# Optimization experiments

Hardware: AMD Instinct MI355X
Metric: run time of the kernel (lower is better)

The kernel has to match this reference:

```python
import jax, jax.numpy as jnp
import numpy as np

MARGIN = 0.5  # init kwarg 'margin'
TWO_N, D = 8192, 256


def setup_inputs() -> dict:
    key = jax.random.key(0)
    k1, k2 = jax.random.split(key)
    embeddings = jax.random.normal(k1, (TWO_N, D), dtype=jnp.float32)
    neg_mask = jax.random.bernoulli(k2, 0.5, (TWO_N, TWO_N))  # bool [2N, 2N]
    return {"embeddings": embeddings, "neg_mask": neg_mask}


def _cdist(x, y):
    # Euclidean pairwise distances via the Gram trick (matches torch.cdist p=2)
    x2 = jnp.sum(x * x, axis=-1)[:, None]
    y2 = jnp.sum(y * y, axis=-1)[None, :]
    sq = jnp.maximum(x2 + y2 - 2.0 * (x @ y.T), 0.0)
    return jnp.sqrt(sq + 1e-12)


def reference(embeddings, neg_mask):
    two_n = embeddings.shape[0]
    n = two_n // 2
    d = _cdist(embeddings, embeddings)  # [2N, 2N]
    # masked sum of exp(margin - d) per anchor row (vectorizes the python loop)
    exp_neg = jnp.where(neg_mask, jnp.exp(MARGIN - d), 0.0)
    row_sums = exp_neg.sum(axis=1)  # [2N]
    idx = jnp.arange(n)
    ap = d[idx, idx + n]  # anchor-positive distances [N]
    j = jnp.log(row_sums[:n] + row_sums[n:]) + ap  # [N]
    # original skips NaN entries before the mean
    valid = ~jnp.isnan(j)
    r2 = jnp.where(valid, jnp.square(jnp.maximum(j, 0.0)), 0.0)
    cnt = jnp.maximum(valid.sum(), 1).astype(r2.dtype)
    loss = r2.sum() / cnt / 2.0
    return loss
```

## Files before the change

kernel.cpp:

```cpp
#include <hip/hip_runtime.h>
#include <hip/hip_bf16.h>
#include <stdint.h>

#define TWO_N  8192
#define NHALF  4096
#define DDIM   256
#define MARGIN 0.5f
#define NTRI   2080

static const size_t OFF_EMB  = 0;
static const size_t OFF_X2   = 4u * 1024 * 1024;
static const size_t OFF_AP   = OFF_X2 + (size_t)TWO_N * 4;
static const size_t OFF_FLAG = OFF_AP + (size_t)NHALF * 4;
static const size_t OFF_PART = OFF_FLAG + 256;
static const size_t OFF_RS   = OFF_PART + 64ull * TWO_N * 4;

typedef __attribute__((ext_vector_type(8))) short bf16x8;
typedef __attribute__((ext_vector_type(4))) float f32x4;

__device__ inline ushort f2bf(float f) {
  uint32_t u = __float_as_uint(f);
  uint32_t r = (u + 0x7FFFu + ((u >> 16) & 1u)) >> 16;
  return (ushort)r;
}
__device__ inline float bf2f(ushort h) { return __uint_as_float((uint32_t)h << 16); }

__device__ inline void gload_lds16(const void* g, void* l) {
  __builtin_amdgcn_global_load_lds(
      (const __attribute__((address_space(1))) uint32_t*)(uintptr_t)g,
      (__attribute__((address_space(3))) uint32_t*)(uint32_t)(uintptr_t)l,
      16, 0, 0);
}

__global__ __launch_bounds__(256) void smv2_prep(
    const float* __restrict__ emb,
    const uint32_t* __restrict__ maskw,
    ushort* __restrict__ emb_bf,
    float* __restrict__ x2,
    int* __restrict__ flag)
{
  const int t = threadIdx.x;
  if (blockIdx.x == 0) {
    __shared__ int sflag;
    if (t == 0) sflag = 0;
    __syncthreads();
    int found = 0;
    #pragma unroll
    for (int k = 0; k < 8; ++k) {
      uint32_t w = maskw[t * 8 + k];
      if (w > 1u && (w & 0xFEFEFEFEu) == 0u) found = 1;
    }
    if (found) atomicOr(&sflag, 1);
    __syncthreads();
    if (t == 0) *flag = sflag;
  }
  const int row  = blockIdx.x * 8 + (t >> 5);
  const int lane = t & 31;
  const float* rp = emb + (size_t)row * DDIM + lane * 8;
  float4 v0 = *(const float4*)(rp);
  float4 v1 = *(const float4*)(rp + 4);
  float vals[8] = {v0.x, v0.y, v0.z, v0.w, v1.x, v1.y, v1.z, v1.w};
  uint32_t packed[4];
  float ss = 0.f;
  #pragma unroll
  for (int k = 0; k < 4; ++k) {
    ushort h0 = f2bf(vals[2 * k]);
    ushort h1 = f2bf(vals[2 * k + 1]);
    packed[k] = (uint32_t)h0 | ((uint32_t)h1 << 16);
    float f0 = bf2f(h0), f1 = bf2f(h1);
    ss += f0 * f0 + f1 * f1;
  }
  *(uint4*)(emb_bf + (size_t)row * DDIM + lane * 8) =
      make_uint4(packed[0], packed[1], packed[2], packed[3]);
  #pragma unroll
  for (int m = 1; m < 32; m <<= 1) ss += __shfl_xor(ss, m);
  if (lane == 0) x2[row] = ss;
}

__global__ __launch_bounds__(512, 6) void smv2_main(
    const ushort* __restrict__ emb_bf,
    const float* __restrict__ x2,
    const uint8_t* __restrict__ mask8,
    const int* __restrict__ flagp,
    float* __restrict__ ap,
    float* __restrict__ partial)
{
  __shared__ char ldsA[128 * 128];
  __shared__ char ldsB[128 * 128];
  __shared__ uint8_t ldsM[128 * 128];
  __shared__ float ldsX[256];

  const int t = threadIdx.x;

  const int bid = blockIdx.x;
  const int idx = (bid & 7) * (NTRI / 8) + (bid >> 3);
  float rf = sqrtf(8.f * (float)idx + 1.f);
  int bx = (int)((rf - 1.f) * 0.5f);
  while ((bx + 1) * (bx + 2) / 2 <= idx) ++bx;
  while (bx * (bx + 1) / 2 > idx) --bx;
  const int by = idx - bx * (bx + 1) / 2;
  const int brow = by * 128;
  const int bcol = bx * 128;
  const bool diag = (bx == by);

  const char* gA = (const char*)(emb_bf + (size_t)brow * DDIM);
  const char* gB = (const char*)(emb_bf + (size_t)bcol * DDIM);

  #pragma unroll
  for (int it = 0; it < 2; ++it) {
    const int dl   = it * 8192 + t * 16;
    const int mrow = dl >> 7;
    const int mc   = dl & 127;
    const int msw  = ((mrow >> 2) & 3) << 5;
    gload_lds16(mask8 + (size_t)(brow + mrow) * TWO_N + bcol + (mc ^ msw), ldsM + dl);
  }
  if (t < 64) {
    const float* src = (t < 32) ? (x2 + brow + t * 4) : (x2 + bcol + (t - 32) * 4);
    gload_lds16(src, (char*)ldsX + t * 16);
  }
  #pragma unroll
  for (int it = 0; it < 2; ++it) {
    const int dl  = it * 8192 + t * 16;
    const int row = dl >> 7;
    const int c   = dl & 127;
    const int cb  = c ^ ((row & 7) << 4);
    gload_lds16(gA + (size_t)row * 512 + cb, ldsA + dl);
    gload_lds16(gB + (size_t)row * 512 + cb, ldsB + dl);
  }
  __syncthreads();

  const int w  = t >> 6;
  const int l  = t & 63;
  const int wr = w >> 2;
  const int wc = w & 3;
  const int cl = l & 15;
  const int kh = l >> 4;
  const int swz = (cl & 7) << 4;

  f32x4 acc[4][2];
  #pragma unroll
  for (int m = 0; m < 4; ++m)
    #pragma unroll
    for (int n = 0; n < 2; ++n) {
      f32x4 z = {0.f, 0.f, 0.f, 0.f};
      acc[m][n] = z;
    }

  #pragma unroll
  for (int p = 0; p < 4; ++p) {
    #pragma unroll
    for (int ks = 0; ks < 2; ++ks) {
      const int kb = ks * 64 + kh * 16;
      bf16x8 a[4], b[2];
      #pragma unroll
      for (int m = 0; m < 4; ++m)
        a[m] = *(const bf16x8*)(ldsA + (wr * 64 + m * 16 + cl) * 128 + (kb ^ swz));
      #pragma unroll
      for (int n = 0; n < 2; ++n)
        b[n] = *(const bf16x8*)(ldsB + (wc * 32 + n * 16 + cl) * 128 + (kb ^ swz));
      #pragma unroll
      for (int m = 0; m < 4; ++m)
        #pragma unroll
        for (int n = 0; n < 2; ++n)
          acc[m][n] = __builtin_amdgcn_mfma_f32_16x16x32_bf16(a[m], b[n], acc[m][n], 0, 0, 0);
    }
    __syncthreads();
    if (p < 3) {
      #pragma unroll
      for (int it = 0; it < 2; ++it) {
        const int dl  = it * 8192 + t * 16;
        const int row = dl >> 7;
        const int c   = dl & 127;
        const int cb  = c ^ ((row & 7) << 4);
        gload_lds16(gA + (size_t)row * 512 + (p + 1) * 128 + cb, ldsA + dl);
        gload_lds16(gB + (size_t)row * 512 + (p + 1) * 128 + cb, ldsB + dl);
      }
      __syncthreads();
    }
  }

  const int isByte = *flagp;
  const uint32_t* maskww = (const uint32_t*)mask8;

  uint32_t m2r[2][4];
  if (!diag && isByte) {
    #pragma unroll
    for (int n = 0; n < 2; ++n) {
      const int gj = bcol + wc * 32 + n * 16 + cl;
      #pragma unroll
      for (int m = 0; m < 4; ++m)
        m2r[n][m] = *(const uint32_t*)(mask8 + (size_t)gj * TWO_N + brow + wr * 64 + m * 16 + kh * 4);
    }
  }

  float* part  = (float*)ldsA;
  float* part2 = (float*)ldsB;
  float cs[2] = {0.f, 0.f};

  #pragma unroll
  for (int m = 0; m < 4; ++m) {
    #pragma unroll
    for (int q = 0; q < 4; ++q) {
      const int lrow = wr * 64 + m * 16 + kh * 4 + q;
      const int gi = brow + lrow;
      const float xi = ldsX[lrow];
      const int msw = kh << 5;
      float rp = 0.f;
      #pragma unroll
      for (int n = 0; n < 2; ++n) {
        const int jc = wc * 32 + n * 16 + cl;
        const int gj = bcol + jc;
        const float g = acc[m][n][q];
        float sq = (gi == gj) ? 0.f : (xi + ldsX[128 + jc] - 2.f * g);
        sq = fmaxf(sq, 0.f) + 1e-12f;
        const float dd = sqrtf(sq);
        if (gj == gi + NHALF && gi < NHALF) ap[gi] = dd;
        const float e = __expf(MARGIN - dd);
        bool mk1;
        if (isByte) mk1 = ldsM[lrow * 128 + (jc ^ msw)] != 0;
        else        mk1 = maskww[(size_t)gi * TWO_N + gj] != 0u;
        rp += mk1 ? e : 0.f;
        if (!diag) {
          bool mk2;
          if (isByte) mk2 = ((m2r[n][m] >> (8 * q)) & 255u) != 0u;
          else        mk2 = maskww[(size_t)gj * TWO_N + gi] != 0u;
          cs[n] += mk2 ? e : 0.f;
        }
      }
      #pragma unroll
      for (int s = 1; s < 16; s <<= 1) rp += __shfl_xor(rp, s);
      if (cl == 0) part[wc * 128 + lrow] = rp;
    }
  }

  if (!diag) {
    #pragma unroll
    for (int n = 0; n < 2; ++n) {
      cs[n] += __shfl_xor(cs[n], 16);
      cs[n] += __shfl_xor(cs[n], 32);
      if (l < 16) part2[wr * 128 + wc * 32 + n * 16 + l] = cs[n];
    }
  }
  __syncthreads();

  if (t < 128) {
    partial[(size_t)bx * TWO_N + brow + t] =
        (part[t] + part[128 + t]) + (part[256 + t] + part[384 + t]);
    if (!diag)
      partial[(size_t)by * TWO_N + bcol + t] = part2[t] + part2[128 + t];
  }
}

__global__ __launch_bounds__(256) void smv2_rowsum(
    const float* __restrict__ partial, float* __restrict__ rs)
{
  const int row = blockIdx.x * 256 + threadIdx.x;
  float s = 0.f;
  #pragma unroll 8
  for (int b = 0; b < 64; ++b) s += partial[(size_t)b * TWO_N + row];
  rs[row] = s;
}

__global__ __launch_bounds__(1024) void smv2_finalize(
    const float* __restrict__ rs, const float* __restrict__ ap,
    float* __restrict__ out)
{
  const int t = threadIdx.x;
  float sum = 0.f, cnt = 0.f;
  for (int i = t; i < NHALF; i += 1024) {
    float rsum = rs[i] + rs[i + NHALF];
    float jv = logf(rsum) + ap[i];
    if (!isnan(jv)) {
      cnt += 1.f;
      float mj = fmaxf(jv, 0.f);
      sum += mj * mj;
    }
  }
  __shared__ float ssum[16], scnt[16];
  #pragma unroll
  for (int s = 32; s >= 1; s >>= 1) {
    sum += __shfl_down(sum, s);
    cnt += __shfl_down(cnt, s);
  }
  const int wid = t >> 6, lid = t & 63;
  if (lid == 0) { ssum[wid] = sum; scnt[wid] = cnt; }
  __syncthreads();
  if (t == 0) {
    float S = 0.f, C = 0.f;
    #pragma unroll
    for (int i = 0; i < 16; ++i) { S += ssum[i]; C += scnt[i]; }
    if (C < 1.f) C = 1.f;
    out[0] = S / C * 0.5f;
  }
}

extern "C" void kernel_launch(void* const* d_in, const int* in_sizes, int n_in,
                              void* d_out, int out_size, void* d_ws, size_t ws_size,
                              hipStream_t stream) {
  const float* emb = (const float*)d_in[0];
  const void* mask = d_in[1];
  char* ws = (char*)d_ws;

  ushort* emb_bf = (ushort*)(ws + OFF_EMB);
  float*  x2     = (float*)(ws + OFF_X2);
  float*  ap     = (float*)(ws + OFF_AP);
  int*    flag   = (int*)(ws + OFF_FLAG);
  float*  part   = (float*)(ws + OFF_PART);
  float*  rs     = (float*)(ws + OFF_RS);

  smv2_prep<<<1024, 256, 0, stream>>>(emb, (const uint32_t*)mask, emb_bf, x2, flag);
  smv2_main<<<NTRI, 512, 0, stream>>>(emb_bf, x2, (const uint8_t*)mask, flag, ap, part);
  smv2_rowsum<<<32, 256, 0, stream>>>(part, rs);
  smv2_finalize<<<1, 1024, 0, stream>>>(rs, ap, (float*)d_out);
}
```

Measured before the change: 455.6 us.

## Pipeline the K-loop with a three-stage LDS ring and explicit vmcnt waits

Replaces the four-step K loop, which loaded a 128-wide chunk and then waited on full barriers, with eight 32-wide phases. The phases use a three-buffer LDS ring filled by direct global-to-LDS loads, with hand-tuned s_waitcnt vmcnt counts so loads overlap the MFMA work. The transposed mask loads move inside the pipeline, and sqrt becomes the raw hardware builtin. The occupancy hint drops from 6 to 4 to leave room for the extra LDS and registers. The risks are lost occupancy, fragile hand-counted waits, and transposed mask loads that now run even on diagonal tiles.

```diff
diff --git a/kernel.cpp b/kernel.cpp
--- a/kernel.cpp
+++ b/kernel.cpp
@@ -31,6 +31,9 @@
       (__attribute__((address_space(3))) uint32_t*)(uint32_t)(uintptr_t)l,
       16, 0, 0);
 }
+
+#define STR2(x) #x
+#define WAITVM(N) asm volatile("s_waitcnt vmcnt(" STR2(N) ")" ::: "memory")
 
 __global__ __launch_bounds__(256) void smv2_prep(
     const float* __restrict__ emb,
@@ -77,7 +80,7 @@
   if (lane == 0) x2[row] = ss;
 }
 
-__global__ __launch_bounds__(512, 6) void smv2_main(
+__global__ __launch_bounds__(512, 4) void smv2_main(
     const ushort* __restrict__ emb_bf,
     const float* __restrict__ x2,
     const uint8_t* __restrict__ mask8,
@@ -85,8 +88,8 @@
     float* __restrict__ ap,
     float* __restrict__ partial)
 {
-  __shared__ char ldsA[128 * 128];
-  __shared__ char ldsB[128 * 128];
+  __shared__ char bufA[3 * 8192];
+  __shared__ char bufB[3 * 8192];
   __shared__ uint8_t ldsM[128 * 128];
   __shared__ float ldsX[256];
 
@@ -106,6 +109,92 @@
   const char* gA = (const char*)(emb_bf + (size_t)brow * DDIM);
   const char* gB = (const char*)(emb_bf + (size_t)bcol * DDIM);
 
+  const int srow = t >> 2;
+  const int scb  = ((t & 3) * 16) ^ (((srow >> 1) & 3) << 4);
+  const size_t gAoff = (size_t)srow * 512 + scb;
+  const size_t gBoff = gAoff;
+  const int ldst = t * 16;
+
+  const int w  = t >> 6;
+  const int l  = t & 63;
+  const int wr = w >> 2;
+  const int wc = w & 3;
+  const int cl = l & 15;
+  const int kh = l >> 4;
+
+  int aoff[4], boff[2];
+  #pragma unroll
+  for (int m = 0; m < 4; ++m) {
+    const int row = wr * 64 + m * 16 + cl;
+    aoff[m] = row * 64 + ((kh * 16) ^ (((row >> 1) & 3) << 4));
+  }
+  #pragma unroll
+  for (int n = 0; n < 2; ++n) {
+    const int row = wc * 32 + n * 16 + cl;
+    boff[n] = row * 64 + ((kh * 16) ^ (((row >> 1) & 3) << 4));
+  }
+
+  f32x4 acc[4][2];
+  #pragma unroll
+  for (int m = 0; m < 4; ++m)
+    #pragma unroll
+    for (int n = 0; n < 2; ++n) {
+      f32x4 z = {0.f, 0.f, 0.f, 0.f};
+      acc[m][n] = z;
+    }
+  uint32_t m2r[2][4];
+
+#define STAGE(Q)                                                            \
+  {                                                                         \
+    gload_lds16(gA + gAoff + (Q) * 64, bufA + ((Q) % 3) * 8192 + ldst);     \
+    gload_lds16(gB + gBoff + (Q) * 64, bufB + ((Q) % 3) * 8192 + ldst);     \
+  }
+
+#define M2LOAD                                                              \
+  {                                                                         \
+    _Pragma("unroll")                                                       \
+    for (int n = 0; n < 2; ++n) {                                           \
+      const int gj = bcol + wc * 32 + n * 16 + cl;                          \
+      _Pragma("unroll")                                                     \
+      for (int m = 0; m < 4; ++m)                                           \
+        m2r[n][m] = *(const uint32_t*)(mask8 + (size_t)gj * TWO_N + brow +  \
+                                       wr * 64 + m * 16 + kh * 4);          \
+    }                                                                       \
+  }
+
+#define COMPUTE(P)                                                          \
+  {                                                                         \
+    const char* ba = bufA + ((P) % 3) * 8192;                               \
+    const char* bb = bufB + ((P) % 3) * 8192;                               \
+    bf16x8 a0 = *(const bf16x8*)(ba + aoff[0]);                             \
+    bf16x8 a1 = *(const bf16x8*)(ba + aoff[1]);                             \
+    bf16x8 a2 = *(const bf16x8*)(ba + aoff[2]);                             \
+    bf16x8 a3 = *(const bf16x8*)(ba + aoff[3]);                             \
+    bf16x8 b0 = *(const bf16x8*)(bb + boff[0]);                             \
+    bf16x8 b1 = *(const bf16x8*)(bb + boff[1]);                             \
+    acc[0][0] = __builtin_amdgcn_mfma_f32_16x16x32_bf16(a0, b0, acc[0][0], 0, 0, 0); \
+    acc[0][1] = __builtin_amdgcn_mfma_f32_16x16x32_bf16(a0, b1, acc[0][1], 0, 0, 0); \
+    acc[1][0] = __builtin_amdgcn_mfma_f32_16x16x32_bf16(a1, b0, acc[1][0], 0, 0, 0); \
+    acc[1][1] = __builtin_amdgcn_mfma_f32_16x16x32_bf16(a1, b1, acc[1][1], 0, 0, 0); \
+    acc[2][0] = __builtin_amdgcn_mfma_f32_16x16x32_bf16(a2, b0, acc[2][0], 0, 0, 0); \
+    acc[2][1] = __builtin_amdgcn_mfma_f32_16x16x32_bf16(a2, b1, acc[2][1], 0, 0, 0); \
+    acc[3][0] = __builtin_amdgcn_mfma_f32_16x16x32_bf16(a3, b0, acc[3][0], 0, 0, 0); \
+    acc[3][1] = __builtin_amdgcn_mfma_f32_16x16x32_bf16(a3, b1, acc[3][1], 0, 0, 0); \
+  }
+
+#define PHASE(P, NW, SQ, DOM2)                                              \
+  {                                                                         \
+    WAITVM(NW);                                                             \
+    __builtin_amdgcn_s_barrier();                                           \
+    __builtin_amdgcn_sched_barrier(0);                                      \
+    if ((SQ) >= 0) STAGE((SQ) < 0 ? 0 : (SQ));                              \
+    if (DOM2) M2LOAD;                                                       \
+    __builtin_amdgcn_sched_barrier(0);                                      \
+    COMPUTE(P);                                                             \
+  }
+
+  STAGE(0);
+  STAGE(1);
   #pragma unroll
   for (int it = 0; it < 2; ++it) {
     const int dl   = it * 8192 + t * 16;
@@ -114,87 +203,25 @@
     const int msw  = ((mrow >> 2) & 3) << 5;
     gload_lds16(mask8 + (size_t)(brow + mrow) * TWO_N + bcol + (mc ^ msw), ldsM + dl);
   }
-  if (t < 64) {
-    const float* src = (t < 32) ? (x2 + brow + t * 4) : (x2 + bcol + (t - 32) * 4);
-    gload_lds16(src, (char*)ldsX + t * 16);
-  }
-  #pragma unroll
-  for (int it = 0; it < 2; ++it) {
-    const int dl  = it * 8192 + t * 16;
-    const int row = dl >> 7;
-    const int c   = dl & 127;
-    const int cb  = c ^ ((row & 7) << 4);
-    gload_lds16(gA + (size_t)row * 512 + cb, ldsA + dl);
-    gload_lds16(gB + (size_t)row * 512 + cb, ldsB + dl);
-  }
-  __syncthreads();
-
-  const int w  = t >> 6;
-  const int l  = t & 63;
-  const int wr = w >> 2;
-  const int wc = w & 3;
-  const int cl = l & 15;
-  const int kh = l >> 4;
-  const int swz = (cl & 7) << 4;
-
-  f32x4 acc[4][2];
-  #pragma unroll
-  for (int m = 0; m < 4; ++m)
-    #pragma unroll
-    for (int n = 0; n < 2; ++n) {
-      f32x4 z = {0.f, 0.f, 0.f, 0.f};
-      acc[m][n] = z;
-    }
-
-  #pragma unroll
-  for (int p = 0; p < 4; ++p) {
-    #pragma unroll
-    for (int ks = 0; ks < 2; ++ks) {
-      const int kb = ks * 64 + kh * 16;
-      bf16x8 a[4], b[2];
-      #pragma unroll
-      for (int m = 0; m < 4; ++m)
-        a[m] = *(const bf16x8*)(ldsA + (wr * 64 + m * 16 + cl) * 128 + (kb ^ swz));
-      #pragma unroll
-      for (int n = 0; n < 2; ++n)
-        b[n] = *(const bf16x8*)(ldsB + (wc * 32 + n * 16 + cl) * 128 + (kb ^ swz));
-      #pragma unroll
-      for (int m = 0; m < 4; ++m)
-        #pragma unroll
-        for (int n = 0; n < 2; ++n)
-          acc[m][n] = __builtin_amdgcn_mfma_f32_16x16x32_bf16(a[m], b[n], acc[m][n], 0, 0, 0);
-    }
-    __syncthreads();
-    if (p < 3) {
-      #pragma unroll
-      for (int it = 0; it < 2; ++it) {
-        const int dl  = it * 8192 + t * 16;
-        const int row = dl >> 7;
-        const int c   = dl & 127;
-        const int cb  = c ^ ((row & 7) << 4);
-        gload_lds16(gA + (size_t)row * 512 + (p + 1) * 128 + cb, ldsA + dl);
-        gload_lds16(gB + (size_t)row * 512 + (p + 1) * 128 + cb, ldsB + dl);
-      }
-      __syncthreads();
-    }
-  }
+  {
+    const float* src = (l < 32) ? (x2 + brow + l * 4) : (x2 + bcol + (l - 32) * 4);
+    gload_lds16(src, (char*)ldsX + l * 16);
+  }
+
+  PHASE(0, 5, 2, 0)
+  PHASE(1, 5, 3, 0)
+  PHASE(2, 2, 4, 0)
+  PHASE(3, 2, 5, 1)
+  PHASE(4, 10, 6, 0)
+  PHASE(5, 10, 7, 0)
+  PHASE(6, 2, -1, 0)
+  PHASE(7, 0, -1, 0)
 
   const int isByte = *flagp;
   const uint32_t* maskww = (const uint32_t*)mask8;
 
-  uint32_t m2r[2][4];
-  if (!diag && isByte) {
-    #pragma unroll
-    for (int n = 0; n < 2; ++n) {
-      const int gj = bcol + wc * 32 + n * 16 + cl;
-      #pragma unroll
-      for (int m = 0; m < 4; ++m)
-        m2r[n][m] = *(const uint32_t*)(mask8 + (size_t)gj * TWO_N + brow + wr * 64 + m * 16 + kh * 4);
-    }
-  }
-
-  float* part  = (float*)ldsA;
-  float* part2 = (float*)ldsB;
+  float* part  = (float*)bufA;
+  float* part2 = (float*)bufB;
   float cs[2] = {0.f, 0.f};
 
   #pragma unroll
@@ -213,7 +240,7 @@
         const float g = acc[m][n][q];
         float sq = (gi == gj) ? 0.f : (xi + ldsX[128 + jc] - 2.f * g);
         sq = fmaxf(sq, 0.f) + 1e-12f;
-        const float dd = sqrtf(sq);
+        const float dd = __builtin_amdgcn_sqrtf(sq);
         if (gj == gi + NHALF && gi < NHALF) ap[gi] = dd;
         const float e = __expf(MARGIN - dd);
         bool mk1;
@@ -249,6 +276,10 @@
     if (!diag)
       partial[(size_t)by * TWO_N + bcol + t] = part2[t] + part2[128 + t];
   }
+#undef PHASE
+#undef COMPUTE
+#undef M2LOAD
+#undef STAGE
 }
 
 __global__ __launch_bounds__(256) void smv2_rowsum(
```

Result: slower. 490.5 us (+7.7%).
